# Kernel optimization log

Hardware: AMD Instinct MI355X
Metric: run time of the kernel (lower is better)

The kernel has to match this reference:

```python
import jax, jax.numpy as jnp
import numpy as np

B, N, C = 16, 2048, 80
CONF_THR = 0.2
NMS_THR = 0.45
OFFSET = 10000.0  # > max box coordinate, separates classes for batched per-class NMS


def setup_inputs() -> dict:
    key = jax.random.key(0)
    k1, k2, k3, k4 = jax.random.split(key, 4)
    cxcy = jax.random.uniform(k1, (B, N, 2)) * 640.0
    wh = jax.random.uniform(k2, (B, N, 2)) * 100.0 + 1.0
    boxes = jnp.concatenate([cxcy - wh / 2, cxcy + wh / 2], axis=-1)  # (x1,y1,x2,y2)
    scores = jax.random.uniform(k3, (B, N, 1))
    classprobs = jax.random.uniform(k4, (B, N, C))
    detection = jnp.concatenate([boxes, scores, classprobs], axis=-1)  # [B,N,85]
    return {"detection": detection}


def _iou_matrix(boxes):
    # boxes: [N,4] -> [N,N] pairwise IoU (torchvision convention, no +1)
    x1, y1, x2, y2 = boxes[:, 0], boxes[:, 1], boxes[:, 2], boxes[:, 3]
    area = jnp.clip(x2 - x1, 0.0) * jnp.clip(y2 - y1, 0.0)
    ix1 = jnp.maximum(x1[:, None], x1[None, :])
    iy1 = jnp.maximum(y1[:, None], y1[None, :])
    ix2 = jnp.minimum(x2[:, None], x2[None, :])
    iy2 = jnp.minimum(y2[:, None], y2[None, :])
    inter = jnp.clip(ix2 - ix1, 0.0) * jnp.clip(iy2 - iy1, 0.0)
    return inter / (area[:, None] + area[None, :] - inter + 1e-7)


def _filter_image(boxes, scores, classprobs, labels):
    # Confidence filter (target_class=None path)
    cand = scores > CONF_THR
    # Sort by descending score, non-candidates last (sort key is non-differentiable)
    sort_key = jnp.where(cand, scores, -jnp.inf)
    order = jnp.argsort(-jax.lax.stop_gradient(sort_key))
    b = boxes[order]
    s = scores[order]
    cp = classprobs[order]
    lb = labels[order]
    cd = cand[order]
    # Per-class NMS via coordinate offset: boxes of different classes never overlap
    ob = b + lb[:, None].astype(b.dtype) * OFFSET
    iou = _iou_matrix(ob)  # [N,N]
    idx = jnp.arange(N)

    def step(active, i):
        keep_i = active[i]
        active = active & ~(keep_i & (iou[i] > NMS_THR) & (idx > i))
        return active, keep_i

    _, keep = jax.lax.scan(step, cd, idx)
    # Final sort by descending score among kept boxes (max_predictions_per_image=-1)
    final_key = jnp.where(keep, jax.lax.stop_gradient(s), -jnp.inf)
    perm = jnp.argsort(-final_key)
    keep_p = keep[perm]
    m = keep_p.astype(b.dtype)
    out_boxes = b[perm] * m[:, None]
    out_scores = s[perm] * m
    out_classprobs = cp[perm] * m
    out_labels = jnp.where(keep_p, lb[perm], 0)
    return out_boxes, out_scores, out_classprobs, out_labels, keep_p


def reference(detection):
    # split_detections
    boxes = detection[..., :4]
    scores = detection[..., 4]
    cp_all = detection[..., 5:]
    classprobs = jnp.max(cp_all, axis=-1)
    labels = jnp.argmax(cp_all, axis=-1)
    ob, osc, ocp, olb, mask = jax.vmap(_filter_image)(boxes, scores, classprobs, labels)
    # Pack float outputs: [B, N, 6] = boxes(4) + score(1) + classprob(1); padded rows are zero
    out = jnp.concatenate([ob, osc[..., None], ocp[..., None]], axis=-1)
    return out, olb, mask
```

## Files before the change

### kernel.cpp

```cpp
#include <hip/hip_runtime.h>

#define BATCH 16
#define NBOX  2048
#define NCLS  80
#define ROWF  85
#define CONF_THRF 0.2f
#define CONF_BITS 0x3E4CCCCDu
#define NMS_THRF  0.45f
#define CAP   128
#define KCAP  128

#define WS_SL   0
#define WS_CP   (WS_SL + BATCH*NBOX*8)
#define WS_KC   (WS_CP + BATCH*NBOX*4)
#define WS_KCLS (WS_KC + (size_t)BATCH*NCLS*KCAP*8)

static __device__ inline unsigned long long shflx64(unsigned long long v, int m) {
  int lo = __shfl_xor((int)(unsigned)(v & 0xffffffffull), m, 64);
  int hi = __shfl_xor((int)(unsigned)(v >> 32), m, 64);
  return ((unsigned long long)(unsigned)hi << 32) | (unsigned)lo;
}

__global__ __launch_bounds__(256) void prep_kernel(const float* __restrict__ det,
                                                   unsigned long long* __restrict__ sl,
                                                   float* __restrict__ cp_ws,
                                                   float* __restrict__ outz) {
  const int tid = threadIdx.x;
  const int lane = tid & 63, wavei = tid >> 6;
  const int sub = lane & 15, grp = lane >> 4;
  const int row = blockIdx.x * 16 + wavei * 4 + grp;

  int gid = blockIdx.x * 256 + tid;
  if (gid < (BATCH * NBOX * 8) / 4)
    ((float4*)outz)[gid] = make_float4(0.f, 0.f, 0.f, 0.f);

  const float* r = det + (size_t)row * ROWF;
  float best = r[5 + sub];
  int bc = sub;
#pragma unroll
  for (int k = 1; k < 5; ++k) {
    float v = r[5 + sub + 16 * k];
    if (v > best) { best = v; bc = sub + 16 * k; }
  }
#pragma unroll
  for (int d = 1; d < 16; d <<= 1) {
    float ov = __shfl_xor(best, d, 16);
    int oc = __shfl_xor(bc, d, 16);
    if (ov > best || (ov == best && oc < bc)) { best = ov; bc = oc; }
  }
  if (sub == 0) {
    sl[row] = ((unsigned long long)__float_as_uint(r[4]) << 32) | (unsigned)bc;
    cp_ws[row] = best;
  }
}

__global__ __launch_bounds__(1024) void nms16_kernel(const float* __restrict__ det,
                                                     const unsigned long long* __restrict__ sl,
                                                     unsigned long long* __restrict__ keptc,
                                                     int* __restrict__ kcls) {
  __shared__ unsigned short cand[16][CAP];
  const int tid = threadIdx.x;
  const int lane = tid & 63, wid = tid >> 6;
  const int j = blockIdx.x * 16 + wid;
  const int img = j / NCLS, c = j - img * NCLS;
  const size_t ibase = (size_t)img * NBOX;
  const unsigned long long* slImg = sl + ibase;
  unsigned short* mycand = cand[wid];

  unsigned long long pf0 = slImg[0 * 64 + lane], pf1 = slImg[1 * 64 + lane];
  unsigned long long pf2 = slImg[2 * 64 + lane], pf3 = slImg[3 * 64 + lane];
  int cnt = 0;
#pragma unroll
  for (int it = 0; it < 32; ++it) {
    unsigned long long cur;
    if ((it & 3) == 0) cur = pf0; else if ((it & 3) == 1) cur = pf1;
    else if ((it & 3) == 2) cur = pf2; else cur = pf3;
    if (it + 4 < 32) {
      unsigned long long nv = slImg[(it + 4) * 64 + lane];
      if ((it & 3) == 0) pf0 = nv; else if ((it & 3) == 1) pf1 = nv;
      else if ((it & 3) == 2) pf2 = nv; else pf3 = nv;
    }
    bool match = ((unsigned)(cur >> 32) > CONF_BITS) && ((unsigned)cur == (unsigned)c);
    unsigned long long mk = __ballot(match);
    if (match) {
      int rk = cnt + __popcll(mk & ((1ull << lane) - 1ull));
      if (rk < CAP) mycand[rk] = (unsigned short)(it * 64 + lane);
    }
    cnt += __popcll(mk);
  }
  int m = cnt < CAP ? cnt : CAP;

  unsigned long long e0 = ~0ull, e1 = ~0ull;
  if (lane < m) {
    int n = mycand[lane];
    e0 = ((unsigned long long)(~(unsigned)(slImg[n] >> 32)) << 32) | (unsigned)n;
  }
  if (lane + 64 < m) {
    int n = mycand[lane + 64];
    e1 = ((unsigned long long)(~(unsigned)(slImg[n] >> 32)) << 32) | (unsigned)n;
  }
  const bool two = (m > 64);
  if (!two) {
#pragma unroll
    for (int k = 2; k <= 64; k <<= 1)
      for (int jj = k >> 1; jj > 0; jj >>= 1) {
        bool amLow = (lane & jj) == 0;
        bool up = ((lane & k) == 0);
        unsigned long long o = shflx64(e0, jj);
        e0 = (up == amLow) ? (e0 < o ? e0 : o) : (e0 > o ? e0 : o);
      }
  } else {
#pragma unroll
    for (int k = 2; k <= 128; k <<= 1)
      for (int jj = k >> 1; jj > 0; jj >>= 1) {
        if (jj == 64) {
          bool up = ((lane & k) == 0);
          if (up ? (e0 > e1) : (e0 < e1)) { unsigned long long t = e0; e0 = e1; e1 = t; }
        } else {
          bool amLow = (lane & jj) == 0;
          bool up0 = ((lane & k) == 0), up1 = (((lane + 64) & k) == 0);
          unsigned long long o0 = shflx64(e0, jj), o1 = shflx64(e1, jj);
          e0 = (up0 == amLow) ? (e0 < o0 ? e0 : o0) : (e0 > o0 ? e0 : o0);
          e1 = (up1 == amLow) ? (e1 < o1 ? e1 : o1) : (e1 > o1 ? e1 : o1);
        }
      }
  }

  const float off = (float)c * 10000.0f;
  bool valid0 = lane < m, valid1 = two && (lane + 64 < m);
  int n0 = (int)((unsigned)e0 & (NBOX - 1));
  int n1 = (int)((unsigned)e1 & (NBOX - 1));
  float x1 = 0, y1 = 0, x2 = 0, y2 = 0, ar = 0;
  if (valid0) {
    const float* rr = det + (ibase + n0) * ROWF;
    x1 = rr[0] + off; y1 = rr[1] + off; x2 = rr[2] + off; y2 = rr[3] + off;
    ar = fmaxf(x2 - x1, 0.0f) * fmaxf(y2 - y1, 0.0f);
  }
  float X1 = 0, Y1 = 0, X2 = 0, Y2 = 0, AR = 0;
  if (valid1) {
    const float* rr = det + (ibase + n1) * ROWF;
    X1 = rr[0] + off; Y1 = rr[1] + off; X2 = rr[2] + off; Y2 = rr[3] + off;
    AR = fmaxf(X2 - X1, 0.0f) * fmaxf(Y2 - Y1, 0.0f);
  }

  unsigned long long keptm0 = 0, und = __ballot(valid0);
  while (und) {
    int i = __ffsll((long long)und) - 1;
    keptm0 |= 1ull << i;
    float kx1 = __shfl(x1, i, 64), ky1 = __shfl(y1, i, 64);
    float kx2 = __shfl(x2, i, 64), ky2 = __shfl(y2, i, 64);
    float kar = __shfl(ar, i, 64);
    float iw = fminf(x2, kx2) - fmaxf(x1, kx1);
    float ih = fminf(y2, ky2) - fmaxf(y1, ky1);
    float inter = fmaxf(iw, 0.0f) * fmaxf(ih, 0.0f);
    float iou = inter / (((kar + ar) - inter) + 1e-7f);
    bool sup = (lane > i) && (iou > NMS_THRF);
    und &= ~__ballot(sup);
    und &= ~(1ull << i);
  }
  unsigned long long keptm1 = 0;
  if (two) {
    bool dead = false;
    unsigned long long km = keptm0;
    while (km) {
      int t = __ffsll((long long)km) - 1; km &= km - 1;
      float kx1 = __shfl(x1, t, 64), ky1 = __shfl(y1, t, 64);
      float kx2 = __shfl(x2, t, 64), ky2 = __shfl(y2, t, 64);
      float kar = __shfl(ar, t, 64);
      float iw = fminf(X2, kx2) - fmaxf(X1, kx1);
      float ih = fminf(Y2, ky2) - fmaxf(Y1, ky1);
      float inter = fmaxf(iw, 0.0f) * fmaxf(ih, 0.0f);
      float iou = inter / (((kar + AR) - inter) + 1e-7f);
      dead |= (iou > NMS_THRF);
    }
    unsigned long long und1 = __ballot(valid1 && !dead);
    while (und1) {
      int i = __ffsll((long long)und1) - 1;
      keptm1 |= 1ull << i;
      float kx1 = __shfl(X1, i, 64), ky1 = __shfl(Y1, i, 64);
      float kx2 = __shfl(X2, i, 64), ky2 = __shfl(Y2, i, 64);
      float kar = __shfl(AR, i, 64);
      float iw = fminf(X2, kx2) - fmaxf(X1, kx1);
      float ih = fminf(Y2, ky2) - fmaxf(Y1, ky1);
      float inter = fmaxf(iw, 0.0f) * fmaxf(ih, 0.0f);
      float iou = inter / (((kar + AR) - inter) + 1e-7f);
      bool sup = (lane > i) && (iou > NMS_THRF);
      und1 &= ~__ballot(sup);
      und1 &= ~(1ull << i);
    }
  }

  unsigned long long* dst = keptc + (size_t)j * KCAP;
  if ((keptm0 >> lane) & 1) {
    int rank = __popcll(keptm0 & ((1ull << lane) - 1ull));
    dst[rank] = (e0 & 0xffffffff00000000ull) | (unsigned)((n0 << 7) | c);
  }
  if (two && ((keptm1 >> lane) & 1)) {
    int rank = __popcll(keptm0) + __popcll(keptm1 & ((1ull << lane) - 1ull));
    dst[rank] = (e1 & 0xffffffff00000000ull) | (unsigned)((n1 << 7) | c);
  }
  if (lane == 0) kcls[j] = __popcll(keptm0) + __popcll(keptm1);
}

__global__ __launch_bounds__(1024) void outr_kernel(const float* __restrict__ det,
                                                    const float* __restrict__ cp_ws,
                                                    const unsigned long long* __restrict__ keptc,
                                                    const int* __restrict__ kcls,
                                                    float* __restrict__ out) {
  __shared__ unsigned long long keys[NBOX];
  __shared__ int offL[NCLS], cntL[NCLS];
  __shared__ int KtotS;
  const int img = blockIdx.x >> 5, seg = blockIdx.x & 31;
  const int tid = threadIdx.x;
  const int lane = tid & 63, wid = tid >> 6;
  const size_t ibase = (size_t)img * NBOX;

  if (wid == 0) {
    int v0 = kcls[img * NCLS + lane];
    int v1 = (lane < NCLS - 64) ? kcls[img * NCLS + 64 + lane] : 0;
    int s0 = v0;
#pragma unroll
    for (int d = 1; d < 64; d <<= 1) { int u = __shfl_up(s0, d, 64); if (lane >= d) s0 += u; }
    int total0 = __shfl(s0, 63, 64);
    int s1 = v1;
#pragma unroll
    for (int d = 1; d < 16; d <<= 1) { int u = __shfl_up(s1, d, 64); if (lane >= d) s1 += u; }
    offL[lane] = s0 - v0; cntL[lane] = v0;
    if (lane < NCLS - 64) { offL[64 + lane] = total0 + s1 - v1; cntL[64 + lane] = v1; }
    if (lane == 15) KtotS = total0 + s1;
  }
  __syncthreads();

  for (int c = wid; c < NCLS; c += 16) {
    int kc = cntL[c], o = offL[c];
    const unsigned long long* src = keptc + (size_t)(img * NCLS + c) * KCAP;
    for (int q = lane; q < kc; q += 64) keys[o + q] = src[q];
  }
  __syncthreads();

  const int K = KtotS;
#pragma unroll
  for (int q = 0; q < 4; ++q) {
    int p = seg * 64 + (wid << 2) + q;
    if (p >= K) continue;
    unsigned long long x = keys[p];
    int cnt = 0;
    {
      int b = offL[lane], n = cntL[lane];
      int lo = 0, hi = n;
      while (lo < hi) { int mid = (lo + hi) >> 1; if (keys[b + mid] < x) lo = mid + 1; else hi = mid; }
      cnt = lo;
    }
    if (lane < NCLS - 64) {
      int b = offL[64 + lane], n = cntL[64 + lane];
      int lo = 0, hi = n;
      while (lo < hi) { int mid = (lo + hi) >> 1; if (keys[b + mid] < x) lo = mid + 1; else hi = mid; }
      cnt += lo;
    }
#pragma unroll
    for (int d = 1; d < 64; d <<= 1) cnt += __shfl_xor(cnt, d, 64);
    if (lane == 0) {
      unsigned meta = (unsigned)x;
      int idx = (meta >> 7) & (NBOX - 1);
      int lb = meta & 127;
      const float* rr = det + (ibase + idx) * ROWF;
      float* orow = out + (ibase + cnt) * 6;
      orow[0] = rr[0]; orow[1] = rr[1]; orow[2] = rr[2]; orow[3] = rr[3];
      orow[4] = __uint_as_float(~(unsigned)(x >> 32));
      orow[5] = cp_ws[ibase + idx];
      out[(size_t)BATCH * NBOX * 6 + ibase + cnt] = (float)lb;
      out[(size_t)BATCH * NBOX * 7 + ibase + cnt] = 1.0f;
    }
  }
}

extern "C" void kernel_launch(void* const* d_in, const int* in_sizes, int n_in,
                              void* d_out, int out_size, void* d_ws, size_t ws_size,
                              hipStream_t stream) {
  const float* det = (const float*)d_in[0];
  float* out = (float*)d_out;
  char* ws = (char*)d_ws;

  unsigned long long* sl = (unsigned long long*)(ws + WS_SL);
  float* cp_ws = (float*)(ws + WS_CP);
  unsigned long long* keptc = (unsigned long long*)(ws + WS_KC);
  int* kcls = (int*)(ws + WS_KCLS);

  prep_kernel<<<BATCH * NBOX / 16, 256, 0, stream>>>(det, sl, cp_ws, out);
  nms16_kernel<<<(BATCH * NCLS) / 16, 1024, 0, stream>>>(det, sl, keptc, kcls);
  outr_kernel<<<BATCH * 32, 1024, 0, stream>>>(det, cp_ws, keptc, kcls, out);
}
```

Before: 37.50 us.

## Bucket candidates per class once per image instead of per-class rescans

Adds a per-image hist kernel that buckets confident boxes into per-class candidate lists using ballot-based ranks and a prefix scan, and writes them to workspace. The NMS kernel then reads its class list directly instead of each wave rescanning all 2048 boxes, and is relaunched with 256-thread blocks (4 jobs per block) to spread work across more blocks. This removes the 80x redundant scan traffic per image. In exchange it adds a kernel launch, a global round trip for the lists, and a serial 80-iteration ballot loop over only 16 blocks.

```diff
diff --git a/kernel.cpp b/kernel.cpp
--- a/kernel.cpp
+++ b/kernel.cpp
@@ -9,11 +9,14 @@
 #define NMS_THRF  0.45f
 #define CAP   128
 #define KCAP  128
+#define JOBS  (BATCH*NCLS)
 
 #define WS_SL   0
 #define WS_CP   (WS_SL + BATCH*NBOX*8)
 #define WS_KC   (WS_CP + BATCH*NBOX*4)
-#define WS_KCLS (WS_KC + (size_t)BATCH*NCLS*KCAP*8)
+#define WS_KCLS (WS_KC + (size_t)JOBS*KCAP*8)
+#define WS_CL   (WS_KCLS + JOBS*4)
+#define WS_CC   (WS_CL + (size_t)JOBS*CAP*2)
 
 static __device__ inline unsigned long long shflx64(unsigned long long v, int m) {
   int lo = __shfl_xor((int)(unsigned)(v & 0xffffffffull), m, 64);
@@ -54,49 +57,76 @@
   }
 }
 
-__global__ __launch_bounds__(1024) void nms16_kernel(const float* __restrict__ det,
-                                                     const unsigned long long* __restrict__ sl,
-                                                     unsigned long long* __restrict__ keptc,
-                                                     int* __restrict__ kcls) {
-  __shared__ unsigned short cand[16][CAP];
-  const int tid = threadIdx.x;
-  const int lane = tid & 63, wid = tid >> 6;
-  const int j = blockIdx.x * 16 + wid;
+__global__ __launch_bounds__(1024) void hist_kernel(const unsigned long long* __restrict__ sl,
+                                                    unsigned short* __restrict__ gclist,
+                                                    int* __restrict__ gccnt) {
+  __shared__ unsigned short clist[NCLS][CAP];
+  __shared__ unsigned short hist[32][NCLS];
+  __shared__ int ccnt[NCLS];
+  const int img = blockIdx.x;
+  const int tid = threadIdx.x, lane = tid & 63, wid = tid >> 6;
+  const unsigned long long* slImg = sl + (size_t)img * NBOX;
+
+  int lrank[2], cls[2];
+#pragma unroll
+  for (int cc = 0; cc < 2; ++cc) {
+    int ch = 2 * wid + cc;
+    unsigned long long kv = slImg[ch * 64 + lane];
+    int c = ((unsigned)(kv >> 32) > CONF_BITS) ? (int)(unsigned)kv : 255;
+    cls[cc] = c; lrank[cc] = 0;
+    for (int cq = 0; cq < NCLS; ++cq) {
+      unsigned long long mask = __ballot(c == cq);
+      if (c == cq) lrank[cc] = __popcll(mask & ((1ull << lane) - 1ull));
+      if (lane == (cq & 63)) hist[ch][cq] = (unsigned short)__popcll(mask);
+    }
+  }
+  __syncthreads();
+  if (tid < NCLS) {
+    int run = 0;
+    for (int k = 0; k < 32; ++k) { int t = hist[k][tid]; hist[k][tid] = (unsigned short)run; run += t; }
+    ccnt[tid] = run < CAP ? run : CAP;
+  }
+  __syncthreads();
+#pragma unroll
+  for (int cc = 0; cc < 2; ++cc) {
+    int c = cls[cc];
+    if (c < NCLS) {
+      int ch = 2 * wid + cc;
+      int rank = (int)hist[ch][c] + lrank[cc];
+      if (rank < CAP) clist[c][rank] = (unsigned short)(ch * 64 + lane);
+    }
+  }
+  __syncthreads();
+  for (int c = wid; c < NCLS; c += 16) {
+    int n = ccnt[c];
+    for (int q = lane; q < n; q += 64)
+      gclist[(size_t)(img * NCLS + c) * CAP + q] = clist[c][q];
+    if (lane == 0) gccnt[img * NCLS + c] = n;
+  }
+}
+
+__global__ __launch_bounds__(256) void nmsb_kernel(const float* __restrict__ det,
+                                                   const unsigned long long* __restrict__ sl,
+                                                   const unsigned short* __restrict__ gclist,
+                                                   const int* __restrict__ gccnt,
+                                                   unsigned long long* __restrict__ keptc,
+                                                   int* __restrict__ kcls) {
+  const int tid = threadIdx.x, lane = tid & 63, wid = tid >> 6;
+  const int j = blockIdx.x * 4 + wid;
   const int img = j / NCLS, c = j - img * NCLS;
   const size_t ibase = (size_t)img * NBOX;
   const unsigned long long* slImg = sl + ibase;
-  unsigned short* mycand = cand[wid];
-
-  unsigned long long pf0 = slImg[0 * 64 + lane], pf1 = slImg[1 * 64 + lane];
-  unsigned long long pf2 = slImg[2 * 64 + lane], pf3 = slImg[3 * 64 + lane];
-  int cnt = 0;
-#pragma unroll
-  for (int it = 0; it < 32; ++it) {
-    unsigned long long cur;
-    if ((it & 3) == 0) cur = pf0; else if ((it & 3) == 1) cur = pf1;
-    else if ((it & 3) == 2) cur = pf2; else cur = pf3;
-    if (it + 4 < 32) {
-      unsigned long long nv = slImg[(it + 4) * 64 + lane];
-      if ((it & 3) == 0) pf0 = nv; else if ((it & 3) == 1) pf1 = nv;
-      else if ((it & 3) == 2) pf2 = nv; else pf3 = nv;
-    }
-    bool match = ((unsigned)(cur >> 32) > CONF_BITS) && ((unsigned)cur == (unsigned)c);
-    unsigned long long mk = __ballot(match);
-    if (match) {
-      int rk = cnt + __popcll(mk & ((1ull << lane) - 1ull));
-      if (rk < CAP) mycand[rk] = (unsigned short)(it * 64 + lane);
-    }
-    cnt += __popcll(mk);
-  }
-  int m = cnt < CAP ? cnt : CAP;
+
+  int m = gccnt[j];
+  if (m > CAP) m = CAP;
 
   unsigned long long e0 = ~0ull, e1 = ~0ull;
   if (lane < m) {
-    int n = mycand[lane];
+    int n = gclist[(size_t)j * CAP + lane];
     e0 = ((unsigned long long)(~(unsigned)(slImg[n] >> 32)) << 32) | (unsigned)n;
   }
   if (lane + 64 < m) {
-    int n = mycand[lane + 64];
+    int n = gclist[(size_t)j * CAP + lane + 64];
     e1 = ((unsigned long long)(~(unsigned)(slImg[n] >> 32)) << 32) | (unsigned)n;
   }
   const bool two = (m > 64);
@@ -285,8 +315,11 @@
   float* cp_ws = (float*)(ws + WS_CP);
   unsigned long long* keptc = (unsigned long long*)(ws + WS_KC);
   int* kcls = (int*)(ws + WS_KCLS);
+  unsigned short* gclist = (unsigned short*)(ws + WS_CL);
+  int* gccnt = (int*)(ws + WS_CC);
 
   prep_kernel<<<BATCH * NBOX / 16, 256, 0, stream>>>(det, sl, cp_ws, out);
-  nms16_kernel<<<(BATCH * NCLS) / 16, 1024, 0, stream>>>(det, sl, keptc, kcls);
+  hist_kernel<<<BATCH, 1024, 0, stream>>>(sl, gclist, gccnt);
+  nmsb_kernel<<<JOBS / 4, 256, 0, stream>>>(det, sl, gclist, gccnt, keptc, kcls);
   outr_kernel<<<BATCH * 32, 1024, 0, stream>>>(det, cp_ws, keptc, kcls, out);
 }
```

Result: slower. 48.23 us (+28.6%).
